# Kernel tuning notes

Hardware: AMD Instinct MI355X
Metric: run time of the kernel (lower is better)

## Reference

```python
import jax, jax.numpy as jnp
import numpy as np

ETA = 0.01
EPSILON = 1e-08


def setup_inputs() -> dict:
    key = jax.random.key(0)
    k1, k2 = jax.random.split(key)
    B, N = 2000000, 16  # batch (time steps), num_assets
    weights = jax.random.uniform(k1, (B, N), dtype=jnp.float32)
    next_returns = jax.random.normal(k2, (B, N), dtype=jnp.float32) * 0.02
    return {"weights": weights, "next_returns": next_returns}


def reference(weights, next_returns):
    # portfolio return per time step: (B,)
    R = jnp.sum(weights * next_returns, axis=1)
    batch_size = R.shape[0]
    eta = jnp.asarray(ETA, R.dtype)
    eps = jnp.asarray(EPSILON, R.dtype)

    def step(carry, R_t):
        A_prev, B_prev = carry
        delta_A = eta * (R_t - A_prev)
        delta_B = eta * (R_t * R_t - B_prev)
        variance = jnp.maximum(B_prev - A_prev * A_prev, eps)
        denom = variance ** 1.5
        D_t = (B_prev * delta_A - 0.5 * A_prev * delta_B) / denom
        return (A_prev + delta_A, B_prev + delta_B), D_t

    init = (jnp.asarray(0.0, R.dtype), jnp.asarray(EPSILON, R.dtype))
    _, D = jax.lax.scan(step, init, R)
    return -jnp.sum(D) / batch_size
```

## Files before the change

### kernel.cpp

```cpp
#include <hip/hip_runtime.h>


#define D_ETA 0.01
#define D_C   (1.0 - D_ETA)
#define D_EPS 1e-8

constexpr int BLOCK = 256;
constexpr int K1_ROWS = 256;
constexpr int CHUNK = 2048;
constexpr int LPT   = CHUNK / BLOCK;

__device__ __forceinline__ float row_R(const float* __restrict__ w,
                                       const float* __restrict__ x,
                                       long long row) {
    const float4* w4 = (const float4*)(w + row * 16);
    const float4* x4 = (const float4*)(x + row * 16);
    double r = 0.0;
#pragma unroll
    for (int q = 0; q < 4; ++q) {
        float4 a = w4[q];
        float4 b = x4[q];
        r += (double)a.x * (double)b.x;
        r += (double)a.y * (double)b.y;
        r += (double)a.z * (double)b.z;
        r += (double)a.w * (double)b.w;
    }
    return (float)r;
}

__global__ __launch_bounds__(BLOCK) void k1_dots(
    const float* __restrict__ w, const float* __restrict__ x, int nrows,
    float* __restrict__ R)
{
    int tid = threadIdx.x;
    int q    = tid & 3;
    int rsub = tid >> 2;
    long long base = (long long)blockIdx.x * K1_ROWS;
    const float4* w4 = (const float4*)w;
    const float4* x4 = (const float4*)x;
#pragma unroll
    for (int it = 0; it < K1_ROWS / 64; ++it) {
        long long row = base + (long long)it * 64 + rsub;
        if (row < nrows) {
            long long f = row * 4 + q;
            float4 a = w4[f];
            float4 b = x4[f];
            double p = (double)a.x * (double)b.x
                     + (double)a.y * (double)b.y
                     + (double)a.z * (double)b.z
                     + (double)a.w * (double)b.w;
            p += __shfl_xor(p, 1, 64);
            p += __shfl_xor(p, 2, 64);
            if (q == 0) R[row] = (float)p;
        }
    }
}

__device__ __forceinline__ void block_scan(double& m, double& sA, double& sB,
                                           double* mS, double* aS, double* bS) {
    int tid = threadIdx.x;
    mS[tid] = m; aS[tid] = sA; bS[tid] = sB;
    __syncthreads();
#pragma unroll
    for (int off = 1; off < BLOCK; off <<= 1) {
        double pm = 1.0, pa = 0.0, pb = 0.0;
        if (tid >= off) { pm = mS[tid - off]; pa = aS[tid - off]; pb = bS[tid - off]; }
        __syncthreads();
        if (tid >= off) {
            sA = m * pa + sA;
            sB = m * pb + sB;
            m  = pm * m;
        }
        mS[tid] = m; aS[tid] = sA; bS[tid] = sB;
        __syncthreads();
    }
}

__device__ __forceinline__ int load_seg(const float* __restrict__ Rws,
                                        const float* __restrict__ w,
                                        const float* __restrict__ x,
                                        long long g0, int nrows, float* rv) {
    long long rem = (long long)nrows - g0;
    int len = rem >= LPT ? LPT : (rem > 0 ? (int)rem : 0);
    if (Rws) {
        if (len == LPT) {
            const float4* Rp = (const float4*)(Rws + g0);
            float4 u = Rp[0], v = Rp[1];
            rv[0]=u.x; rv[1]=u.y; rv[2]=u.z; rv[3]=u.w;
            rv[4]=v.x; rv[5]=v.y; rv[6]=v.z; rv[7]=v.w;
        } else {
            for (int k = 0; k < len; ++k) rv[k] = Rws[g0 + k];
        }
    } else {
        for (int k = 0; k < len; ++k) rv[k] = row_R(w, x, g0 + k);
    }
    return len;
}

__global__ __launch_bounds__(BLOCK) void k2_partials(
    const float* __restrict__ Rws,
    const float* __restrict__ w, const float* __restrict__ x, int nrows,
    double* __restrict__ blkM, double* __restrict__ blkA, double* __restrict__ blkB)
{
    __shared__ double mS[BLOCK], aS[BLOCK], bS[BLOCK];
    int tid = threadIdx.x;
    long long g0 = (long long)blockIdx.x * CHUNK + (long long)tid * LPT;
    float rv[LPT];
    int len = load_seg(Rws, w, x, g0, nrows, rv);

    double m = 1.0, sA = 0.0, sB = 0.0;
    for (int k = 0; k < len; ++k) {
        double r = (double)rv[k];
        sA = D_C * sA + D_ETA * r;
        sB = D_C * sB + D_ETA * (r * r);
        m *= D_C;
    }
    block_scan(m, sA, sB, mS, aS, bS);
    if (tid == BLOCK - 1) {
        blkM[blockIdx.x] = m;
        blkA[blockIdx.x] = sA;
        blkB[blockIdx.x] = sB;
    }
}

__global__ __launch_bounds__(BLOCK) void k3_scan(
    int nb,
    const double* __restrict__ blkM, const double* __restrict__ blkA,
    const double* __restrict__ blkB,
    double* __restrict__ A0, double* __restrict__ B0)
{
    __shared__ double mS[BLOCK], aS[BLOCK], bS[BLOCK];
    int tid = threadIdx.x;
    int K = (nb + BLOCK - 1) / BLOCK;
    int g0 = tid * K;
    int g1 = g0 + K; if (g1 > nb) g1 = nb;

    double m = 1.0, sA = 0.0, sB = 0.0;
    for (int g = g0; g < g1; ++g) {
        double mg = blkM[g], ag = blkA[g], bg = blkB[g];
        sA = mg * sA + ag;
        sB = mg * sB + bg;
        m *= mg;
    }
    block_scan(m, sA, sB, mS, aS, bS);

    double em = 1.0, ea = 0.0, eb = 0.0;
    if (tid > 0) { em = mS[tid - 1]; ea = aS[tid - 1]; eb = bS[tid - 1]; }
    double A = ea;
    double B = em * D_EPS + eb;
    for (int g = g0; g < g1; ++g) {
        A0[g] = A; B0[g] = B;
        double mg = blkM[g], ag = blkA[g], bg = blkB[g];
        A = mg * A + ag;
        B = mg * B + bg;
    }
}

__global__ __launch_bounds__(BLOCK) void k4_dsum(
    const float* __restrict__ Rws,
    const float* __restrict__ w, const float* __restrict__ x, int nrows,
    const double* __restrict__ A0, const double* __restrict__ B0,
    double* __restrict__ bsum)
{
    __shared__ double mS[BLOCK], aS[BLOCK], bS[BLOCK];
    __shared__ double wsum[BLOCK / 64];
    int tid = threadIdx.x;
    long long g0 = (long long)blockIdx.x * CHUNK + (long long)tid * LPT;
    float rv[LPT];
    int len = load_seg(Rws, w, x, g0, nrows, rv);

    double m = 1.0, sA = 0.0, sB = 0.0;
    for (int k = 0; k < len; ++k) {
        double r = (double)rv[k];
        sA = D_C * sA + D_ETA * r;
        sB = D_C * sB + D_ETA * (r * r);
        m *= D_C;
    }
    block_scan(m, sA, sB, mS, aS, bS);

    double em = 1.0, ea = 0.0, eb = 0.0;
    if (tid > 0) { em = mS[tid - 1]; ea = aS[tid - 1]; eb = bS[tid - 1]; }
    double A = em * A0[blockIdx.x] + ea;
    double B = em * B0[blockIdx.x] + eb;

    double dsum = 0.0;
    for (int k = 0; k < len; ++k) {
        double r = (double)rv[k];
        double dA = D_ETA * (r - A);
        double dB = D_ETA * (r * r - B);
        double var = B - A * A;
        if (var < D_EPS) var = D_EPS;
        double denom = var * sqrt(var);
        dsum += (B * dA - 0.5 * A * dB) / denom;
        A += dA;
        B += dB;
    }

#pragma unroll
    for (int off = 32; off > 0; off >>= 1) dsum += __shfl_down(dsum, off, 64);
    if ((tid & 63) == 0) wsum[tid >> 6] = dsum;
    __syncthreads();
    if (tid == 0) bsum[blockIdx.x] = wsum[0] + wsum[1] + wsum[2] + wsum[3];
}

__global__ __launch_bounds__(BLOCK) void k5_final(
    const double* __restrict__ bsum, int nb, int nrows, float* __restrict__ out)
{
    __shared__ double sh[BLOCK / 64];
    int tid = threadIdx.x;
    double s = 0.0;
    for (int i = tid; i < nb; i += BLOCK) s += bsum[i];
#pragma unroll
    for (int off = 32; off > 0; off >>= 1) s += __shfl_down(s, off, 64);
    if ((tid & 63) == 0) sh[tid >> 6] = s;
    __syncthreads();
    if (tid == 0) out[0] = (float)(-(sh[0] + sh[1] + sh[2] + sh[3]) / (double)nrows);
}

extern "C" void kernel_launch(void* const* d_in, const int* in_sizes, int n_in,
                              void* d_out, int out_size, void* d_ws, size_t ws_size,
                              hipStream_t stream)
{
    const float* w = (const float*)d_in[0];
    const float* x = (const float*)d_in[1];
    int nrows = in_sizes[0] / 16;
    int nb  = (nrows + CHUNK - 1) / CHUNK;
    int nb1 = (nrows + K1_ROWS - 1) / K1_ROWS;

    char* ws = (char*)d_ws;
    double* blkM = (double*)(ws + 64);
    double* blkA = blkM + nb;
    double* blkB = blkA + nb;
    double* A0   = blkB + nb;
    double* B0   = A0 + nb;
    double* bsum = B0 + nb;
    size_t off = 64 + (size_t)6 * nb * sizeof(double);
    off = (off + 255) & ~(size_t)255;
    float* Rws = nullptr;
    if (ws_size >= off + (size_t)nrows * sizeof(float))
        Rws = (float*)(ws + off);

    if (Rws)
        k1_dots<<<nb1, BLOCK, 0, stream>>>(w, x, nrows, Rws);
    k2_partials<<<nb, BLOCK, 0, stream>>>(Rws, w, x, nrows, blkM, blkA, blkB);
    k3_scan<<<1, BLOCK, 0, stream>>>(nb, blkM, blkA, blkB, A0, B0);
    k4_dsum<<<nb, BLOCK, 0, stream>>>(Rws, w, x, nrows, A0, B0, bsum);
    k5_final<<<1, BLOCK, 0, stream>>>(bsum, nb, nrows, (float*)d_out);
}
```

Before: 285.8 us.

## Fuse all stages into one cooperative kernel with grid syncs

Replaces the five-kernel pipeline with a single cooperative kernel. Each block computes its rows' portfolio returns straight into LDS, scans them locally, and publishes its block partials. After a grid sync, each block rescans the preceding block partials to get its starting state, then computes its D sum; a second grid sync lets block 0 do the final reduction. This removes the global round trip of R and the extra launches, at the cost of a redundant partial rescan per block and a dependence on all blocks fitting co-resident.

```diff
diff --git a/kernel.cpp b/kernel.cpp
--- a/kernel.cpp
+++ b/kernel.cpp
@@ -1,4 +1,7 @@
 #include <hip/hip_runtime.h>
+#include <hip/hip_cooperative_groups.h>
+
+namespace cg = cooperative_groups;
 
 
 #define D_ETA 0.01
@@ -9,6 +12,166 @@
 constexpr int K1_ROWS = 256;
 constexpr int CHUNK = 2048;
 constexpr int LPT   = CHUNK / BLOCK;
+constexpr int MAX_COOP_BLOCKS = 1024;
+
+__device__ __forceinline__ void block_scan(double& m, double& sA, double& sB,
+                                           double* mS, double* aS, double* bS) {
+    int tid = threadIdx.x;
+    mS[tid] = m; aS[tid] = sA; bS[tid] = sB;
+    __syncthreads();
+#pragma unroll
+    for (int off = 1; off < BLOCK; off <<= 1) {
+        double pm = 1.0, pa = 0.0, pb = 0.0;
+        if (tid >= off) { pm = mS[tid - off]; pa = aS[tid - off]; pb = bS[tid - off]; }
+        __syncthreads();
+        if (tid >= off) {
+            sA = m * pa + sA;
+            sB = m * pb + sB;
+            m  = pm * m;
+        }
+        mS[tid] = m; aS[tid] = sA; bS[tid] = sB;
+        __syncthreads();
+    }
+}
+
+__global__ __launch_bounds__(BLOCK, 4) void k_all(
+    const float* __restrict__ w, const float* __restrict__ x, int nrows,
+    double* __restrict__ blkM, double* __restrict__ blkA, double* __restrict__ blkB,
+    double* __restrict__ bsum, float* __restrict__ out)
+{
+    __shared__ float  Rlds[CHUNK];
+    __shared__ double mS[BLOCK], aS[BLOCK], bS[BLOCK];
+    __shared__ double wred[BLOCK / 64];
+
+    const int tid = threadIdx.x;
+    const int b   = blockIdx.x;
+    const int nb  = gridDim.x;
+    const long long base = (long long)b * CHUNK;
+
+    {
+        const int q = tid & 3, rsub = tid >> 2;
+        const float4* w4 = (const float4*)w;
+        const float4* x4 = (const float4*)x;
+        if (base + CHUNK <= (long long)nrows) {
+            const long long f0 = (base + rsub) * 4 + q;
+#pragma unroll
+            for (int p0 = 0; p0 < 32; p0 += 8) {
+                float4 av[8], bv[8];
+#pragma unroll
+                for (int u = 0; u < 8; ++u) {
+                    long long f = f0 + (long long)(p0 + u) * 256;
+                    av[u] = w4[f];
+                    bv[u] = x4[f];
+                }
+#pragma unroll
+                for (int u = 0; u < 8; ++u) {
+                    double p = (double)av[u].x * bv[u].x
+                             + (double)av[u].y * bv[u].y
+                             + (double)av[u].z * bv[u].z
+                             + (double)av[u].w * bv[u].w;
+                    p += __shfl_xor(p, 1, 64);
+                    p += __shfl_xor(p, 2, 64);
+                    if (q == 0) Rlds[(p0 + u) * 64 + rsub] = (float)p;
+                }
+            }
+        } else {
+            for (int p = 0; p < 32; ++p) {
+                long long row = base + (long long)p * 64 + rsub;
+                double pd = 0.0;
+                if (row < (long long)nrows) {
+                    long long f = row * 4 + q;
+                    float4 a = w4[f], c = x4[f];
+                    pd = (double)a.x * c.x + (double)a.y * c.y
+                       + (double)a.z * c.z + (double)a.w * c.w;
+                }
+                pd += __shfl_xor(pd, 1, 64);
+                pd += __shfl_xor(pd, 2, 64);
+                if (q == 0) Rlds[p * 64 + rsub] = (float)pd;
+            }
+        }
+    }
+    __syncthreads();
+
+    float rv[LPT];
+    {
+        const float4* Rp = (const float4*)&Rlds[tid * LPT];
+        float4 u0 = Rp[0], u1 = Rp[1];
+        rv[0] = u0.x; rv[1] = u0.y; rv[2] = u0.z; rv[3] = u0.w;
+        rv[4] = u1.x; rv[5] = u1.y; rv[6] = u1.z; rv[7] = u1.w;
+    }
+    long long g0 = base + (long long)tid * LPT;
+    long long rem = (long long)nrows - g0;
+    int len = rem >= LPT ? LPT : (rem > 0 ? (int)rem : 0);
+
+    double m = 1.0, sA = 0.0, sB = 0.0;
+    for (int k = 0; k < len; ++k) {
+        double r = (double)rv[k];
+        sA = D_C * sA + D_ETA * r;
+        sB = D_C * sB + D_ETA * (r * r);
+        m *= D_C;
+    }
+    block_scan(m, sA, sB, mS, aS, bS);
+    if (tid == BLOCK - 1) { blkM[b] = m; blkA[b] = sA; blkB[b] = sB; }
+    double em = 1.0, ea = 0.0, eb = 0.0;
+    if (tid > 0) { em = mS[tid - 1]; ea = aS[tid - 1]; eb = bS[tid - 1]; }
+
+    cg::this_grid().sync();
+
+    double A, B;
+    {
+        double cm = 1.0, ca = 0.0, cb = 0.0;
+        const int nseg = b;
+        const int K = (nseg + BLOCK - 1) / BLOCK;
+        int s0 = tid * K;
+        int s1 = s0 + K; if (s1 > nseg) s1 = nseg;
+        for (int g = s0; g < s1; ++g) {
+            double mg = blkM[g], ag = blkA[g], bg = blkB[g];
+            ca = mg * ca + ag;
+            cb = mg * cb + bg;
+            cm *= mg;
+        }
+        block_scan(cm, ca, cb, mS, aS, bS);
+        double M  = mS[BLOCK - 1];
+        double SA = aS[BLOCK - 1];
+        double SB = bS[BLOCK - 1];
+        double Astart = SA;
+        double Bstart = M * D_EPS + SB;
+        A = em * Astart + ea;
+        B = em * Bstart + eb;
+    }
+
+    double dsum = 0.0;
+    for (int k = 0; k < len; ++k) {
+        double r = (double)rv[k];
+        double dA = D_ETA * (r - A);
+        double dB = D_ETA * (r * r - B);
+        double var = B - A * A;
+        if (var < D_EPS) var = D_EPS;
+        double denom = var * sqrt(var);
+        dsum += (B * dA - 0.5 * A * dB) / denom;
+        A += dA;
+        B += dB;
+    }
+#pragma unroll
+    for (int off = 32; off > 0; off >>= 1) dsum += __shfl_down(dsum, off, 64);
+    if ((tid & 63) == 0) wred[tid >> 6] = dsum;
+    __syncthreads();
+    if (tid == 0) bsum[b] = wred[0] + wred[1] + wred[2] + wred[3];
+
+    cg::this_grid().sync();
+
+    if (b == 0) {
+        double s = 0.0;
+        for (int i = tid; i < nb; i += BLOCK) s += bsum[i];
+#pragma unroll
+        for (int off = 32; off > 0; off >>= 1) s += __shfl_down(s, off, 64);
+        if ((tid & 63) == 0) wred[tid >> 6] = s;
+        __syncthreads();
+        if (tid == 0)
+            out[0] = (float)(-(wred[0] + wred[1] + wred[2] + wred[3]) / (double)nrows);
+    }
+}
+
 
 __device__ __forceinline__ float row_R(const float* __restrict__ w,
                                        const float* __restrict__ x,
@@ -53,26 +216,6 @@
             p += __shfl_xor(p, 2, 64);
             if (q == 0) R[row] = (float)p;
         }
-    }
-}
-
-__device__ __forceinline__ void block_scan(double& m, double& sA, double& sB,
-                                           double* mS, double* aS, double* bS) {
-    int tid = threadIdx.x;
-    mS[tid] = m; aS[tid] = sA; bS[tid] = sB;
-    __syncthreads();
-#pragma unroll
-    for (int off = 1; off < BLOCK; off <<= 1) {
-        double pm = 1.0, pa = 0.0, pb = 0.0;
-        if (tid >= off) { pm = mS[tid - off]; pa = aS[tid - off]; pb = bS[tid - off]; }
-        __syncthreads();
-        if (tid >= off) {
-            sA = m * pa + sA;
-            sB = m * pb + sB;
-            m  = pm * m;
-        }
-        mS[tid] = m; aS[tid] = sA; bS[tid] = sB;
-        __syncthreads();
     }
 }
 
@@ -234,6 +377,20 @@
     double* A0   = blkB + nb;
     double* B0   = A0 + nb;
     double* bsum = B0 + nb;
+
+    if (nb >= 1 && nb <= MAX_COOP_BLOCKS &&
+        ws_size >= 64 + (size_t)6 * nb * sizeof(double)) {
+        float* outp = (float*)d_out;
+        void* args[] = { (void*)&w, (void*)&x, (void*)&nrows,
+                         (void*)&blkM, (void*)&blkA, (void*)&blkB,
+                         (void*)&bsum, (void*)&outp };
+        hipError_t e = hipLaunchCooperativeKernel((const void*)k_all,
+                                                  dim3(nb), dim3(BLOCK),
+                                                  args, 0, stream);
+        if (e == hipSuccess) return;
+        (void)hipGetLastError();
+    }
+
     size_t off = 64 + (size_t)6 * nb * sizeof(double);
     off = (off + 255) & ~(size_t)255;
     float* Rws = nullptr;
```

After: 477.1 us. 66.9% more time.

## Fuse row dot products with per-chunk partial scan in one kernel

Applied to the files above, without the earlier changes.

Merges the dot-product kernel and the chunk-partial kernel into one. Each block computes its chunk's portfolio returns into LDS, writes them to the workspace for the later pass, and runs the local affine scan directly from LDS. This drops one kernel launch and the global write-then-read of R between those two stages. Loads are batched eight at a time behind a scheduling barrier to raise memory-level parallelism, at the cost of more registers and LDS per block.

```diff
diff --git a/kernel.cpp b/kernel.cpp
--- a/kernel.cpp
+++ b/kernel.cpp
@@ -6,55 +6,10 @@
 #define D_EPS 1e-8
 
 constexpr int BLOCK = 256;
-constexpr int K1_ROWS = 256;
 constexpr int CHUNK = 2048;
 constexpr int LPT   = CHUNK / BLOCK;
-
-__device__ __forceinline__ float row_R(const float* __restrict__ w,
-                                       const float* __restrict__ x,
-                                       long long row) {
-    const float4* w4 = (const float4*)(w + row * 16);
-    const float4* x4 = (const float4*)(x + row * 16);
-    double r = 0.0;
-#pragma unroll
-    for (int q = 0; q < 4; ++q) {
-        float4 a = w4[q];
-        float4 b = x4[q];
-        r += (double)a.x * (double)b.x;
-        r += (double)a.y * (double)b.y;
-        r += (double)a.z * (double)b.z;
-        r += (double)a.w * (double)b.w;
-    }
-    return (float)r;
-}
-
-__global__ __launch_bounds__(BLOCK) void k1_dots(
-    const float* __restrict__ w, const float* __restrict__ x, int nrows,
-    float* __restrict__ R)
-{
-    int tid = threadIdx.x;
-    int q    = tid & 3;
-    int rsub = tid >> 2;
-    long long base = (long long)blockIdx.x * K1_ROWS;
-    const float4* w4 = (const float4*)w;
-    const float4* x4 = (const float4*)x;
-#pragma unroll
-    for (int it = 0; it < K1_ROWS / 64; ++it) {
-        long long row = base + (long long)it * 64 + rsub;
-        if (row < nrows) {
-            long long f = row * 4 + q;
-            float4 a = w4[f];
-            float4 b = x4[f];
-            double p = (double)a.x * (double)b.x
-                     + (double)a.y * (double)b.y
-                     + (double)a.z * (double)b.z
-                     + (double)a.w * (double)b.w;
-            p += __shfl_xor(p, 1, 64);
-            p += __shfl_xor(p, 2, 64);
-            if (q == 0) R[row] = (float)p;
-        }
-    }
-}
+constexpr int PASSES = CHUNK / 64;
+constexpr int BATCH  = 8;
 
 __device__ __forceinline__ void block_scan(double& m, double& sA, double& sB,
                                            double* mS, double* aS, double* bS) {
@@ -74,6 +29,115 @@
         mS[tid] = m; aS[tid] = sA; bS[tid] = sB;
         __syncthreads();
     }
+}
+
+__global__ __launch_bounds__(BLOCK, 4) void k1_fused(
+    const float* __restrict__ w, const float* __restrict__ x, int nrows,
+    float* __restrict__ Rws,
+    double* __restrict__ blkM, double* __restrict__ blkA, double* __restrict__ blkB)
+{
+    __shared__ float  Rlds[CHUNK];
+    __shared__ double mS[BLOCK], aS[BLOCK], bS[BLOCK];
+
+    const int tid = threadIdx.x;
+    const int b   = blockIdx.x;
+    const long long base = (long long)b * CHUNK;
+    const int q    = tid & 3;
+    const int rsub = tid >> 2;
+    const float4* w4 = (const float4*)w;
+    const float4* x4 = (const float4*)x;
+
+    const bool full = (base + CHUNK <= (long long)nrows);
+
+    if (full) {
+        const long long f0 = base * 4 + tid;
+        for (int p0 = 0; p0 < PASSES; p0 += BATCH) {
+            float4 av[BATCH], bv[BATCH];
+#pragma unroll
+            for (int u = 0; u < BATCH; ++u) {
+                const long long f = f0 + (long long)(p0 + u) * 256;
+                av[u] = w4[f];
+                bv[u] = x4[f];
+            }
+            __builtin_amdgcn_sched_barrier(0);
+#pragma unroll
+            for (int u = 0; u < BATCH; ++u) {
+                double p = (double)av[u].x * bv[u].x
+                         + (double)av[u].y * bv[u].y
+                         + (double)av[u].z * bv[u].z
+                         + (double)av[u].w * bv[u].w;
+                p += __shfl_xor(p, 1, 64);
+                p += __shfl_xor(p, 2, 64);
+                if (q == 0) Rlds[(p0 + u) * 64 + rsub] = (float)p;
+            }
+        }
+    } else {
+        for (int p = 0; p < PASSES; ++p) {
+            long long row = base + (long long)p * 64 + rsub;
+            double pd = 0.0;
+            if (row < (long long)nrows) {
+                long long f = row * 4 + q;
+                float4 a = w4[f], c = x4[f];
+                pd = (double)a.x * c.x + (double)a.y * c.y
+                   + (double)a.z * c.z + (double)a.w * c.w;
+            }
+            pd += __shfl_xor(pd, 1, 64);
+            pd += __shfl_xor(pd, 2, 64);
+            if (q == 0) Rlds[p * 64 + rsub] = (float)pd;
+        }
+    }
+    __syncthreads();
+
+    float rv[LPT];
+    {
+        const float4* Rp = (const float4*)&Rlds[tid * LPT];
+        float4 u0 = Rp[0], u1 = Rp[1];
+        rv[0] = u0.x; rv[1] = u0.y; rv[2] = u0.z; rv[3] = u0.w;
+        rv[4] = u1.x; rv[5] = u1.y; rv[6] = u1.z; rv[7] = u1.w;
+    }
+    long long g0 = base + (long long)tid * LPT;
+    long long rem = (long long)nrows - g0;
+    int len = rem >= LPT ? LPT : (rem > 0 ? (int)rem : 0);
+
+    if (len == LPT) {
+        float4* Rp = (float4*)(Rws + g0);
+        Rp[0] = make_float4(rv[0], rv[1], rv[2], rv[3]);
+        Rp[1] = make_float4(rv[4], rv[5], rv[6], rv[7]);
+    } else {
+        for (int k = 0; k < len; ++k) Rws[g0 + k] = rv[k];
+    }
+
+    double m = 1.0, sA = 0.0, sB = 0.0;
+    for (int k = 0; k < len; ++k) {
+        double r = (double)rv[k];
+        sA = D_C * sA + D_ETA * r;
+        sB = D_C * sB + D_ETA * (r * r);
+        m *= D_C;
+    }
+    block_scan(m, sA, sB, mS, aS, bS);
+    if (tid == BLOCK - 1) {
+        blkM[b] = m;
+        blkA[b] = sA;
+        blkB[b] = sB;
+    }
+}
+
+__device__ __forceinline__ float row_R(const float* __restrict__ w,
+                                       const float* __restrict__ x,
+                                       long long row) {
+    const float4* w4 = (const float4*)(w + row * 16);
+    const float4* x4 = (const float4*)(x + row * 16);
+    double r = 0.0;
+#pragma unroll
+    for (int q = 0; q < 4; ++q) {
+        float4 a = w4[q];
+        float4 b = x4[q];
+        r += (double)a.x * (double)b.x;
+        r += (double)a.y * (double)b.y;
+        r += (double)a.z * (double)b.z;
+        r += (double)a.w * (double)b.w;
+    }
+    return (float)r;
 }
 
 __device__ __forceinline__ int load_seg(const float* __restrict__ Rws,
@@ -225,7 +289,6 @@
     const float* x = (const float*)d_in[1];
     int nrows = in_sizes[0] / 16;
     int nb  = (nrows + CHUNK - 1) / CHUNK;
-    int nb1 = (nrows + K1_ROWS - 1) / K1_ROWS;
 
     char* ws = (char*)d_ws;
     double* blkM = (double*)(ws + 64);
@@ -234,15 +297,18 @@
     double* A0   = blkB + nb;
     double* B0   = A0 + nb;
     double* bsum = B0 + nb;
+
     size_t off = 64 + (size_t)6 * nb * sizeof(double);
     off = (off + 255) & ~(size_t)255;
     float* Rws = nullptr;
     if (ws_size >= off + (size_t)nrows * sizeof(float))
         Rws = (float*)(ws + off);
 
-    if (Rws)
-        k1_dots<<<nb1, BLOCK, 0, stream>>>(w, x, nrows, Rws);
-    k2_partials<<<nb, BLOCK, 0, stream>>>(Rws, w, x, nrows, blkM, blkA, blkB);
+    if (Rws) {
+        k1_fused<<<nb, BLOCK, 0, stream>>>(w, x, nrows, Rws, blkM, blkA, blkB);
+    } else {
+        k2_partials<<<nb, BLOCK, 0, stream>>>(Rws, w, x, nrows, blkM, blkA, blkB);
+    }
     k3_scan<<<1, BLOCK, 0, stream>>>(nb, blkM, blkA, blkB, A0, B0);
     k4_dsum<<<nb, BLOCK, 0, stream>>>(Rws, w, x, nrows, A0, B0, bsum);
     k5_final<<<1, BLOCK, 0, stream>>>(bsum, nb, nrows, (float*)d_out);
```

Measured after the change: 286.8 us. Within noise of the previous version (+0.4%).
